# Performance work log

Hardware: AMD Instinct MI355X
Metric: run time of the kernel (lower is better)

The kernel has to match this reference:

```python
import jax, jax.numpy as jnp
import numpy as np

N, E, B = 50000, 800000, 1000
NODE_DIN, BB_DOUT, DHID, K = 32, 64, 64, 3
GLOB_DIN, EMBED_DIN = 64, 64
CIN = BB_DOUT + NODE_DIN  # 96


def setup_inputs() -> dict:
    key = jax.random.key(0)
    ks = jax.random.split(key, 24)

    def w(k, shape, fan_in):
        return jax.random.normal(k, shape, jnp.float32) / np.float32(np.sqrt(fan_in))

    inp = dict(
        x=jax.random.normal(ks[0], (N, NODE_DIN), jnp.float32),
        u=jax.random.normal(ks[1], (B, GLOB_DIN), jnp.float32),
        z=jax.random.normal(ks[2], (N, BB_DOUT), jnp.float32),
        edge_index=jax.random.randint(ks[3], (2, E), 0, N),
        edge_weight=jax.random.uniform(ks[4], (E,), jnp.float32),
        batch=jnp.sort(jax.random.randint(ks[5], (N,), 0, B)),
        batch_size=B,
        prev_h=jax.random.normal(ks[6], (N, DHID), jnp.float32),
    )
    # six ChebConvs of GConvGRU: x-convs take CIN, h-convs take DHID; all output DHID
    for i, nm in enumerate(["xz", "hz", "xr", "hr", "xh", "hh"]):
        cin = CIN if nm[0] == "x" else DHID
        inp[f"W{nm}"] = w(ks[7 + 2 * i], (K, cin, DHID), cin * K)
        inp[f"b{nm}"] = jnp.zeros((DHID,), jnp.float32)
    inp["Wg"] = w(ks[20], (GLOB_DIN, EMBED_DIN), GLOB_DIN)
    inp["bg"] = jnp.zeros((EMBED_DIN,), jnp.float32)
    return inp


def _cheb(xin, W, b, src, dst, w_norm, n):
    """ChebConv with sym norm, lambda_max=2 -> L_hat = -D^-1/2 A D^-1/2 (diag cancels)."""
    def prop(t):  # L_hat @ t  ([N,C])
        return -jax.ops.segment_sum(w_norm[:, None] * t[src], dst, num_segments=n)

    out = xin @ W[0] + b
    tx_prev = xin
    tx = None
    if W.shape[0] > 1:
        tx = prop(xin)
        out = out + tx @ W[1]
    for k in range(2, W.shape[0]):
        tx_new = 2.0 * prop(tx) - tx_prev
        out = out + tx_new @ W[k]
        tx_prev, tx = tx, tx_new
    return out


def reference(x, u, z, edge_index, edge_weight, batch, batch_size, prev_h,
              Wxz, bxz, Whz, bhz, Wxr, bxr, Whr, bhr, Wxh, bxh, Whh, bhh, Wg, bg):
    n = x.shape[0]
    src, dst = edge_index[0], edge_index[1]
    deg = jax.ops.segment_sum(edge_weight, src, num_segments=n)
    deg_safe = jnp.where(deg > 0, deg, 1.0)
    dinv = jnp.where(deg > 0, jax.lax.rsqrt(deg_safe), 0.0)
    w_norm = dinv[src] * edge_weight * dinv[dst]

    xin = jnp.concatenate([z, x], axis=-1)  # [N, CIN]
    Z = jax.nn.sigmoid(_cheb(xin, Wxz, bxz, src, dst, w_norm, n)
                       + _cheb(prev_h, Whz, bhz, src, dst, w_norm, n))
    R = jax.nn.sigmoid(_cheb(xin, Wxr, bxr, src, dst, w_norm, n)
                       + _cheb(prev_h, Whr, bhr, src, dst, w_norm, n))
    Ht = jnp.tanh(_cheb(xin, Wxh, bxh, src, dst, w_norm, n)
                  + _cheb(prev_h * R, Whh, bhh, src, dst, w_norm, n))
    h = Z * prev_h + (1.0 - Z) * Ht

    graph_emb = jax.ops.segment_sum(z, batch, num_segments=batch_size)  # [B, BB_DOUT]
    global_emb = jax.nn.relu(u @ Wg + bg)                                # [B, EMBED_DIN]
    fused = jnp.concatenate([graph_emb, global_emb], axis=-1)           # [B, 128]
    return fused, h
```

## Files before the change

kernel.cpp:

```cpp
#include <hip/hip_runtime.h>

#define NN 50000
#define EE 800000
#define BB 1000
#define NB 196
#define NR 5
#define RS 10496
#define NC 32
#define CHUNK 25000

#define BUILD2 31250
#define PACK2 408
#define FINBLKS 782

typedef unsigned short u16;
typedef __attribute__((ext_vector_type(8))) short bf16x8;
typedef __attribute__((ext_vector_type(4))) float f32x4;

static __device__ __forceinline__ u16 f2b(float f) {
    union { float f; unsigned u; } v;
    v.f = f;
    unsigned r = v.u + 0x7fffu + ((v.u >> 16) & 1u);
    return (u16)(r >> 16);
}

static __device__ __forceinline__ float b2f(short s) {
    union { unsigned u; float f; } c;
    c.u = ((unsigned)(u16)s) << 16;
    return c.f;
}

__global__ __launch_bounds__(512) void k_hist(
    const int* __restrict__ src, const int* __restrict__ dst,
    const float* __restrict__ ew, float* __restrict__ deg_p,
    int* __restrict__ cnt_p, int* __restrict__ ctr) {
    __shared__ float sdeg[RS];
    __shared__ unsigned scnt2[RS / 2];
    if (blockIdx.x == 0 && threadIdx.x == 0) atomicExch(ctr, 0);
    int r = blockIdx.x % NR;
    int c = blockIdx.x / NR;
    int base = r * RS;
    for (int i = threadIdx.x; i < RS; i += 512) sdeg[i] = 0.f;
    for (int i = threadIdx.x; i < RS / 2; i += 512) scnt2[i] = 0u;
    __syncthreads();
    int e0 = c * CHUNK;
    for (int j = threadIdx.x; j < CHUNK; j += 512) {
        int e = e0 + j;
        int s = src[e], d = dst[e];
        int sl = s - base, dl = d - base;
        if ((unsigned)sl < RS) atomicAdd(&sdeg[sl], ew[e]);
        if ((unsigned)dl < RS) atomicAdd(&scnt2[dl >> 1], (dl & 1) ? 65536u : 1u);
    }
    __syncthreads();
    int lim = (NN - base < RS) ? (NN - base) : RS;
    for (int i = threadIdx.x; i < lim; i += 512) {
        deg_p[(size_t)c * NN + base + i] = sdeg[i];
        cnt_p[(size_t)c * NN + base + i] = (int)((scnt2[i >> 1] >> ((i & 1) * 16)) & 0xffffu);
    }
}

__global__ __launch_bounds__(256) void k_scan_build(
    const int* __restrict__ cnt_p, const float* __restrict__ deg_p,
    int* __restrict__ cnt, int* __restrict__ cbase, float* __restrict__ dinv,
    int* __restrict__ bsum, int* __restrict__ ctr,
    const float* __restrict__ z, const float* __restrict__ x,
    const float* __restrict__ ph, u16* __restrict__ A0,
    const float* __restrict__ Wxz, const float* __restrict__ Wxr,
    const float* __restrict__ Wxh, const float* __restrict__ Whz,
    const float* __restrict__ Whr, const float* __restrict__ Whh,
    u16* __restrict__ Wp, u16* __restrict__ W3p) {
    if (blockIdx.x >= NB) {
        int bid = blockIdx.x - NB;
        if (bid < BUILD2) {
            int i = bid * 256 + threadIdx.x;
            int n = i / 160, c = i - n * 160;
            float v;
            if (c < 64) v = z[n * 64 + c];
            else if (c < 96) v = x[n * 32 + (c - 64)];
            else v = ph[n * 64 + (c - 96)];
            A0[(size_t)n * 160 + c] = f2b(v);
        } else {
            int idx = (bid - BUILD2) * 256 + threadIdx.x;
            if (idx < 15 * 12 * 512) {
                int j = idx & 7, l = (idx >> 3) & 63;
                int ct = (idx >> 9) % 12, s = (idx >> 9) / 12;
                int k = 32 * s + (l >> 4) * 8 + j;
                int g = ct >> 2;
                int c = 16 * (ct & 3) + (l & 15);
                int lvl = k / 160, kk = k - lvl * 160;
                float val;
                if (kk < 96) {
                    const float* W = (g == 0) ? Wxz : ((g == 1) ? Wxr : Wxh);
                    val = W[(lvl * 96 + kk) * 64 + c];
                } else if (g == 2) {
                    val = 0.f;
                } else {
                    const float* W = (g == 0) ? Whz : Whr;
                    val = W[(lvl * 64 + (kk - 96)) * 64 + c];
                }
                Wp[idx] = f2b(val);
            } else {
                int i2 = idx - 15 * 12 * 512;
                int j = i2 & 7, l = (i2 >> 3) & 63;
                int ct = (i2 >> 9) & 3, s = i2 >> 11;
                int k = 32 * s + (l >> 4) * 8 + j;
                int ki = k >> 6, kr = k & 63;
                int c = 16 * ct + (l & 15);
                W3p[i2] = f2b(Whh[(ki * 64 + kr) * 64 + c]);
            }
        }
        return;
    }
    __shared__ int s[256];
    int b = blockIdx.x;
    int i = b * 256 + threadIdx.x;
    int v = 0;
    float d = 0.f;
    if (i < NN) {
#pragma unroll
        for (int p = 0; p < NC; p++) v += cnt_p[(size_t)p * NN + i];
#pragma unroll
        for (int p = 0; p < NC; p++) d += deg_p[(size_t)p * NN + i];
        cnt[i] = v;
    }
    s[threadIdx.x] = v;
    __syncthreads();
    for (int off = 1; off < 256; off <<= 1) {
        int t = (threadIdx.x >= off) ? s[threadIdx.x - off] : 0;
        __syncthreads();
        s[threadIdx.x] += t;
        __syncthreads();
    }
    int incl = s[threadIdx.x];
    if (threadIdx.x == 255) atomicExch(&bsum[b], s[255]);
    __threadfence();
    if (threadIdx.x == 0) {
        atomicAdd(ctr, 1);
        while (atomicAdd(ctr, 0) < NB) __builtin_amdgcn_s_sleep(8);
    }
    __syncthreads();
    __threadfence();
    int pv = (threadIdx.x < b) ? atomicAdd(&bsum[threadIdx.x], 0) : 0;
    s[threadIdx.x] = pv;
    __syncthreads();
    for (int off = 128; off > 0; off >>= 1) {
        if (threadIdx.x < off) s[threadIdx.x] += s[threadIdx.x + off];
        __syncthreads();
    }
    int prefix = s[0];
    if (i < NN) {
        int run = prefix + incl - v;
        dinv[i] = d > 0.f ? rsqrtf(d) : 0.f;
#pragma unroll
        for (int c = 0; c < NC; c++) {
            cbase[(size_t)c * NN + i] = run;
            run += cnt_p[(size_t)c * NN + i];
        }
    }
}

__global__ __launch_bounds__(512) void k_scatter_rank(
    const int* __restrict__ src, const int* __restrict__ dst,
    const float* __restrict__ ew, const float* __restrict__ dinv,
    const int* __restrict__ cbase, uint2* __restrict__ csr8) {
    __shared__ unsigned rank2[RS / 2];
    int r = blockIdx.x % NR;
    int c = blockIdx.x / NR;
    int base = r * RS;
    for (int i = threadIdx.x; i < RS / 2; i += 512) rank2[i] = 0u;
    __syncthreads();
    int e0 = c * CHUNK;
    for (int j = threadIdx.x; j < CHUNK; j += 512) {
        int e = e0 + j;
        int d = dst[e];
        int dl = d - base;
        if ((unsigned)dl < RS) {
            int s = src[e];
            unsigned old = atomicAdd(&rank2[dl >> 1], (dl & 1) ? 65536u : 1u);
            int rank = (int)((old >> ((dl & 1) * 16)) & 0xffffu);
            int pos = cbase[(size_t)c * NN + d] + rank;
            float w = dinv[s] * ew[e] * dinv[d];
            csr8[pos] = make_uint2((unsigned)s, __float_as_uint(w));
        }
    }
}

template <int C, int SCALE, bool HB, int BS, int INS, int OUTS>
__global__ __launch_bounds__(BS) void k_pull(
    const u16* __restrict__ in, const u16* __restrict__ base, u16* __restrict__ out,
    const uint2* __restrict__ csr8, const int* __restrict__ row_ptr,
    const int* __restrict__ cnt) {
    constexpr int TPR = C / 16;
    int tid = blockIdx.x * BS + threadIdx.x;
    int r = tid / TPR;
    int c16 = (tid - r * TPR) * 16;
    if (r >= NN) return;
    int s0 = row_ptr[r], n = cnt[r];
    float acc[16];
#pragma unroll
    for (int k = 0; k < 16; k++) acc[k] = 0.f;
    const u16* inp = in + c16;
    uint2 e = (n > 0) ? csr8[s0] : make_uint2(0u, 0u);
    for (int j = 0; j < n; j++) {
        uint2 ec = e;
        if (j + 1 < n) e = csr8[s0 + j + 1];
        float w = __uint_as_float(ec.y);
        const u16* p = inp + (size_t)ec.x * INS;
        bf16x8 v0 = *(const bf16x8*)(p);
        bf16x8 v1 = *(const bf16x8*)(p + 8);
#pragma unroll
        for (int k = 0; k < 8; k++) {
            acc[k] += w * b2f(v0[k]);
            acc[8 + k] += w * b2f(v1[k]);
        }
    }
    const float sc = -(float)SCALE;
    float o[16];
    if (HB) {
        const u16* bp = base + (size_t)r * INS + c16;
        bf16x8 b0 = *(const bf16x8*)(bp);
        bf16x8 b1 = *(const bf16x8*)(bp + 8);
#pragma unroll
        for (int k = 0; k < 8; k++) {
            o[k] = sc * acc[k] - b2f(b0[k]);
            o[8 + k] = sc * acc[8 + k] - b2f(b1[k]);
        }
    } else {
#pragma unroll
        for (int k = 0; k < 16; k++) o[k] = sc * acc[k];
    }
    bf16x8 p0, p1;
#pragma unroll
    for (int k = 0; k < 8; k++) {
        p0[k] = (short)f2b(o[k]);
        p1[k] = (short)f2b(o[8 + k]);
    }
    u16* op = out + (size_t)r * OUTS + c16;
    *(bf16x8*)(op) = p0;
    *(bf16x8*)(op + 8) = p1;
}

__global__ __launch_bounds__(256) void k_gates_mfma(
    const u16* __restrict__ A0, const u16* __restrict__ A1, const u16* __restrict__ A2,
    const u16* __restrict__ Wp,
    const float* __restrict__ bxz, const float* __restrict__ bhz,
    const float* __restrict__ bxr, const float* __restrict__ bhr,
    const float* __restrict__ bxh,
    u16* __restrict__ Zb16, u16* __restrict__ Hx16, u16* __restrict__ A3) {
    int wv = (blockIdx.x * 256 + threadIdx.x) >> 6;
    int lane = threadIdx.x & 63;
    int r0 = wv * 16;
    if (r0 >= NN) return;
    int q = lane >> 4, j0 = lane & 15;

    f32x4 acc[12];
#pragma unroll
    for (int i = 0; i < 12; i++) acc[i] = (f32x4){0.f, 0.f, 0.f, 0.f};

    size_t rofs = (size_t)(r0 + j0) * 160 + q * 8;
    const u16* arow[3] = {A0 + rofs, A1 + rofs, A2 + rofs};
#pragma unroll
    for (int s = 0; s < 15; s++) {
        bf16x8 a = *(const bf16x8*)(arow[s / 5] + 32 * (s % 5));
        const u16* bp = Wp + (size_t)(s * 12) * 512 + lane * 8;
#pragma unroll
        for (int ct = 0; ct < 12; ct++) {
            bf16x8 b = *(const bf16x8*)(bp + ct * 512);
            acc[ct] = __builtin_amdgcn_mfma_f32_16x16x32_bf16(a, b, acc[ct], 0, 0, 0);
        }
    }

#pragma unroll
    for (int ct = 0; ct < 4; ct++) {
        int j = 16 * ct + j0;
        float bz = bxz[j] + bhz[j];
        float br = bxr[j] + bhr[j];
        float bh = bxh[j];
#pragma unroll
        for (int reg = 0; reg < 4; reg++) {
            int r = r0 + q * 4 + reg;
            size_t i = (size_t)r * 64 + j;
            float zp = acc[ct][reg] + bz;
            float rp = acc[ct + 4][reg] + br;
            float hp = acc[ct + 8][reg] + bh;
            float zv = 1.f / (1.f + expf(-zp));
            float rv = 1.f / (1.f + expf(-rp));
            float phv = b2f((short)A0[(size_t)r * 160 + 96 + j]);
            Zb16[i] = f2b(zv);
            Hx16[i] = f2b(hp);
            A3[(size_t)r * 192 + j] = f2b(rv * phv);
        }
    }
}

__global__ __launch_bounds__(256) void k_final_tail(
    const u16* __restrict__ A3, const u16* __restrict__ W3p,
    const float* __restrict__ bhh, const u16* __restrict__ Hx16,
    const u16* __restrict__ Zb16, const u16* __restrict__ A0,
    float* __restrict__ outh,
    const float* __restrict__ z, const int* __restrict__ batch,
    const float* __restrict__ u, const float* __restrict__ Wg,
    const float* __restrict__ bg, float* __restrict__ outF) {
    if (blockIdx.x >= FINBLKS) {
        int b = ((blockIdx.x - FINBLKS) * 256 + threadIdx.x) >> 6;
        int lane = threadIdx.x & 63;
        if (b >= BB) return;
        int lo = 0, hi = NN;
        while (lo < hi) {
            int m = (lo + hi) >> 1;
            if (batch[m] < b) lo = m + 1; else hi = m;
        }
        int start = lo;
        hi = NN;
        while (lo < hi) {
            int m = (lo + hi) >> 1;
            if (batch[m] < b + 1) lo = m + 1; else hi = m;
        }
        int end = lo;
        float acc = 0.f;
        for (int n = start; n < end; n++) acc += z[(size_t)n * 64 + lane];
        float g = bg[lane];
        const float* ur = u + (size_t)b * 64;
        for (int k = 0; k < 64; k++) g += ur[k] * Wg[k * 64 + lane];
        g = fmaxf(g, 0.f);
        outF[(size_t)b * 128 + lane] = acc;
        outF[(size_t)b * 128 + 64 + lane] = g;
        return;
    }
    int wv = (blockIdx.x * 256 + threadIdx.x) >> 6;
    int lane = threadIdx.x & 63;
    int r0 = wv * 16;
    if (r0 >= NN) return;
    int q = lane >> 4, j0 = lane & 15;

    f32x4 acc[4];
#pragma unroll
    for (int i = 0; i < 4; i++) acc[i] = (f32x4){0.f, 0.f, 0.f, 0.f};

    const u16* arow = A3 + (size_t)(r0 + j0) * 192 + q * 8;
#pragma unroll
    for (int s = 0; s < 6; s++) {
        bf16x8 a = *(const bf16x8*)(arow + 32 * s);
        const u16* bp = W3p + (size_t)(s * 4) * 512 + lane * 8;
#pragma unroll
        for (int ct = 0; ct < 4; ct++) {
            bf16x8 b = *(const bf16x8*)(bp + ct * 512);
            acc[ct] = __builtin_amdgcn_mfma_f32_16x16x32_bf16(a, b, acc[ct], 0, 0, 0);
        }
    }

#pragma unroll
    for (int ct = 0; ct < 4; ct++) {
        int j = 16 * ct + j0;
        float bh = bhh[j];
#pragma unroll
        for (int reg = 0; reg < 4; reg++) {
            int r = r0 + q * 4 + reg;
            size_t i = (size_t)r * 64 + j;
            float ht = tanhf(b2f((short)Hx16[i]) + acc[ct][reg] + bh);
            float zv = b2f((short)Zb16[i]);
            float phv = b2f((short)A0[(size_t)r * 160 + 96 + j]);
            outh[i] = zv * phv + (1.f - zv) * ht;
        }
    }
}

extern "C" void kernel_launch(void* const* d_in, const int* in_sizes, int n_in,
                              void* d_out, int out_size, void* d_ws, size_t ws_size,
                              hipStream_t stream) {
    const float* x  = (const float*)d_in[0];
    const float* u  = (const float*)d_in[1];
    const float* z  = (const float*)d_in[2];
    const int*   ei = (const int*)d_in[3];
    const float* ew = (const float*)d_in[4];
    const int* batch = (const int*)d_in[5];
    const float* ph = (const float*)d_in[7];
    const float *Wxz = (const float*)d_in[8],  *bxz = (const float*)d_in[9];
    const float *Whz = (const float*)d_in[10], *bhz = (const float*)d_in[11];
    const float *Wxr = (const float*)d_in[12], *bxr = (const float*)d_in[13];
    const float *Whr = (const float*)d_in[14], *bhr = (const float*)d_in[15];
    const float *Wxh = (const float*)d_in[16], *bxh = (const float*)d_in[17];
    const float *Whh = (const float*)d_in[18], *bhh = (const float*)d_in[19];
    const float *Wg  = (const float*)d_in[20], *bg  = (const float*)d_in[21];
    const int* src = ei;
    const int* dst = ei + EE;

    char* wsb = (char*)d_ws;
    size_t o = 0;
    auto alloc = [&](size_t bytes) {
        void* p = wsb + o;
        o += (bytes + 255) & ~(size_t)255;
        return p;
    };
    float* deg_p = (float*)alloc((size_t)NC * NN * 4);
    int*   cnt_p = (int*)alloc((size_t)NC * NN * 4);
    int*   cnt   = (int*)alloc(NN * 4);
    int*   cbase = (int*)alloc((size_t)NC * NN * 4);
    float* dinv  = (float*)alloc(NN * 4);
    int*   bsum  = (int*)alloc(256 * 4);
    int*   ctr   = (int*)alloc(256);
    uint2* csr8  = (uint2*)alloc((size_t)EE * 8);
    u16*   Zb16  = (u16*)alloc((size_t)NN * 64 * 2);
    u16*   Hx16  = (u16*)alloc((size_t)NN * 64 * 2);
    u16*   A0    = (u16*)alloc((size_t)NN * 160 * 2);
    u16*   A1    = (u16*)alloc((size_t)NN * 160 * 2);
    u16*   A2    = (u16*)alloc((size_t)NN * 160 * 2);
    u16*   A3    = (u16*)alloc((size_t)NN * 192 * 2);
    u16*   Wp    = (u16*)alloc(15 * 12 * 512 * 2);
    u16*   W3p   = (u16*)alloc(6 * 4 * 512 * 2);

    float* outF = (float*)d_out;
    float* outH = outF + (size_t)BB * 128;

    const int BLK = 256;
    const int gPull160 = (NN + 31) / 32;
    const int gPull64 = (NN + 63) / 64;
    const int gTail = (BB * 64 + BLK - 1) / BLK;
    int* row_ptr = cbase;

    k_hist<<<NR * NC, 512, 0, stream>>>(src, dst, ew, deg_p, cnt_p, ctr);

    k_scan_build<<<NB + BUILD2 + PACK2, 256, 0, stream>>>(
        cnt_p, deg_p, cnt, cbase, dinv, bsum, ctr,
        z, x, ph, A0, Wxz, Wxr, Wxh, Whz, Whr, Whh, Wp, W3p);

    k_scatter_rank<<<NR * NC, 512, 0, stream>>>(src, dst, ew, dinv, cbase, csr8);

    k_pull<160, 1, false, 320, 160, 160><<<gPull160, 320, 0, stream>>>(
        A0, nullptr, A1, csr8, row_ptr, cnt);
    k_pull<160, 2, true, 320, 160, 160><<<gPull160, 320, 0, stream>>>(
        A1, A0, A2, csr8, row_ptr, cnt);

    k_gates_mfma<<<FINBLKS, BLK, 0, stream>>>(A0, A1, A2, Wp, bxz, bhz, bxr, bhr, bxh,
                                              Zb16, Hx16, A3);

    k_pull<64, 1, false, 256, 192, 192><<<gPull64, 256, 0, stream>>>(
        A3, nullptr, A3 + 64, csr8, row_ptr, cnt);
    k_pull<64, 2, true, 256, 192, 192><<<gPull64, 256, 0, stream>>>(
        A3 + 64, A3, A3 + 128, csr8, row_ptr, cnt);

    k_final_tail<<<FINBLKS + gTail, BLK, 0, stream>>>(A3, W3p, bhh, Hx16, Zb16, A0, outH,
                                                      z, batch, u, Wg, bg, outF);
}
```

Measured before the change: 458.3 us.

## Fold Chebyshev recurrence into packed weights and split scan from build

The Chebyshev T2 = 2*L*T1 - T0 term is folded into the weights: W0' = W0 - W2 and W2' = 2*W2, so the second pull stores L*T1 directly and skips reading the base tensor and the fused scale/subtract. The combined scan/build kernel is split into a separate build kernel with 512-thread blocks and a separate scan kernel. The scan now keeps per-chunk counts in registers instead of reloading them from memory. The split adds one kernel launch, and dropping the co-scheduled build work may change how the spin barrier in the scan behaves. Folding the weights changes bf16 rounding slightly.

```diff
diff --git a/kernel.cpp b/kernel.cpp
--- a/kernel.cpp
+++ b/kernel.cpp
@@ -9,8 +9,8 @@
 #define NC 32
 #define CHUNK 25000
 
-#define BUILD2 31250
-#define PACK2 408
+#define BUILDBLKS 15625
+#define PACKBLKS 204
 #define FINBLKS 782
 
 typedef unsigned short u16;
@@ -59,68 +59,80 @@
     }
 }
 
-__global__ __launch_bounds__(256) void k_scan_build(
-    const int* __restrict__ cnt_p, const float* __restrict__ deg_p,
-    int* __restrict__ cnt, int* __restrict__ cbase, float* __restrict__ dinv,
-    int* __restrict__ bsum, int* __restrict__ ctr,
+__global__ __launch_bounds__(512) void k_build(
     const float* __restrict__ z, const float* __restrict__ x,
     const float* __restrict__ ph, u16* __restrict__ A0,
     const float* __restrict__ Wxz, const float* __restrict__ Wxr,
     const float* __restrict__ Wxh, const float* __restrict__ Whz,
     const float* __restrict__ Whr, const float* __restrict__ Whh,
     u16* __restrict__ Wp, u16* __restrict__ W3p) {
-    if (blockIdx.x >= NB) {
-        int bid = blockIdx.x - NB;
-        if (bid < BUILD2) {
-            int i = bid * 256 + threadIdx.x;
-            int n = i / 160, c = i - n * 160;
-            float v;
-            if (c < 64) v = z[n * 64 + c];
-            else if (c < 96) v = x[n * 32 + (c - 64)];
-            else v = ph[n * 64 + (c - 96)];
-            A0[(size_t)n * 160 + c] = f2b(v);
+    int bid = blockIdx.x;
+    if (bid < BUILDBLKS) {
+        int i = bid * 512 + threadIdx.x;
+        int n = i / 160, c = i - n * 160;
+        float v;
+        if (c < 64) v = z[n * 64 + c];
+        else if (c < 96) v = x[n * 32 + (c - 64)];
+        else v = ph[n * 64 + (c - 96)];
+        A0[(size_t)n * 160 + c] = f2b(v);
+        return;
+    }
+    int idx = (bid - BUILDBLKS) * 512 + threadIdx.x;
+    if (idx < 15 * 12 * 512) {
+        int j = idx & 7, l = (idx >> 3) & 63;
+        int ct = (idx >> 9) % 12, s = (idx >> 9) / 12;
+        int k = 32 * s + (l >> 4) * 8 + j;
+        int g = ct >> 2;
+        int c = 16 * (ct & 3) + (l & 15);
+        int lvl = k / 160, kk = k - lvl * 160;
+        float val;
+        if (kk < 96) {
+            const float* W = (g == 0) ? Wxz : ((g == 1) ? Wxr : Wxh);
+            if (lvl == 0)      val = W[kk * 64 + c] - W[(192 + kk) * 64 + c];
+            else if (lvl == 1) val = W[(96 + kk) * 64 + c];
+            else               val = 2.f * W[(192 + kk) * 64 + c];
+        } else if (g == 2) {
+            val = 0.f;
         } else {
-            int idx = (bid - BUILD2) * 256 + threadIdx.x;
-            if (idx < 15 * 12 * 512) {
-                int j = idx & 7, l = (idx >> 3) & 63;
-                int ct = (idx >> 9) % 12, s = (idx >> 9) / 12;
-                int k = 32 * s + (l >> 4) * 8 + j;
-                int g = ct >> 2;
-                int c = 16 * (ct & 3) + (l & 15);
-                int lvl = k / 160, kk = k - lvl * 160;
-                float val;
-                if (kk < 96) {
-                    const float* W = (g == 0) ? Wxz : ((g == 1) ? Wxr : Wxh);
-                    val = W[(lvl * 96 + kk) * 64 + c];
-                } else if (g == 2) {
-                    val = 0.f;
-                } else {
-                    const float* W = (g == 0) ? Whz : Whr;
-                    val = W[(lvl * 64 + (kk - 96)) * 64 + c];
-                }
-                Wp[idx] = f2b(val);
-            } else {
-                int i2 = idx - 15 * 12 * 512;
-                int j = i2 & 7, l = (i2 >> 3) & 63;
-                int ct = (i2 >> 9) & 3, s = i2 >> 11;
-                int k = 32 * s + (l >> 4) * 8 + j;
-                int ki = k >> 6, kr = k & 63;
-                int c = 16 * ct + (l & 15);
-                W3p[i2] = f2b(Whh[(ki * 64 + kr) * 64 + c]);
-            }
-        }
-        return;
-    }
+            const float* W = (g == 0) ? Whz : Whr;
+            int kh = kk - 96;
+            if (lvl == 0)      val = W[kh * 64 + c] - W[(128 + kh) * 64 + c];
+            else if (lvl == 1) val = W[(64 + kh) * 64 + c];
+            else               val = 2.f * W[(128 + kh) * 64 + c];
+        }
+        Wp[idx] = f2b(val);
+    } else {
+        int i2 = idx - 15 * 12 * 512;
+        int j = i2 & 7, l = (i2 >> 3) & 63;
+        int ct = (i2 >> 9) & 3, s = i2 >> 11;
+        int k = 32 * s + (l >> 4) * 8 + j;
+        int ki = k >> 6, kr = k & 63;
+        int c = 16 * ct + (l & 15);
+        float val;
+        if (ki == 0)      val = Whh[kr * 64 + c] - Whh[(128 + kr) * 64 + c];
+        else if (ki == 1) val = Whh[(64 + kr) * 64 + c];
+        else              val = 2.f * Whh[(128 + kr) * 64 + c];
+        W3p[i2] = f2b(val);
+    }
+}
+
+__global__ __launch_bounds__(256) void k_scan(
+    const int* __restrict__ cnt_p, const float* __restrict__ deg_p,
+    int* __restrict__ cnt, int* __restrict__ cbase, float* __restrict__ dinv,
+    int* __restrict__ bsum, int* __restrict__ ctr) {
     __shared__ int s[256];
     int b = blockIdx.x;
     int i = b * 256 + threadIdx.x;
+    int cp[NC];
     int v = 0;
     float d = 0.f;
     if (i < NN) {
 #pragma unroll
-        for (int p = 0; p < NC; p++) v += cnt_p[(size_t)p * NN + i];
-#pragma unroll
-        for (int p = 0; p < NC; p++) d += deg_p[(size_t)p * NN + i];
+        for (int p = 0; p < NC; p++) {
+            cp[p] = cnt_p[(size_t)p * NN + i];
+            v += cp[p];
+            d += deg_p[(size_t)p * NN + i];
+        }
         cnt[i] = v;
     }
     s[threadIdx.x] = v;
@@ -154,7 +166,7 @@
 #pragma unroll
         for (int c = 0; c < NC; c++) {
             cbase[(size_t)c * NN + i] = run;
-            run += cnt_p[(size_t)c * NN + i];
+            run += cp[c];
         }
     }
 }
@@ -185,9 +197,9 @@
     }
 }
 
-template <int C, int SCALE, bool HB, int BS, int INS, int OUTS>
+template <int C, int BS, int INS, int OUTS>
 __global__ __launch_bounds__(BS) void k_pull(
-    const u16* __restrict__ in, const u16* __restrict__ base, u16* __restrict__ out,
+    const u16* __restrict__ in, u16* __restrict__ out,
     const uint2* __restrict__ csr8, const int* __restrict__ row_ptr,
     const int* __restrict__ cnt) {
     constexpr int TPR = C / 16;
@@ -214,26 +226,11 @@
             acc[8 + k] += w * b2f(v1[k]);
         }
     }
-    const float sc = -(float)SCALE;
-    float o[16];
-    if (HB) {
-        const u16* bp = base + (size_t)r * INS + c16;
-        bf16x8 b0 = *(const bf16x8*)(bp);
-        bf16x8 b1 = *(const bf16x8*)(bp + 8);
-#pragma unroll
-        for (int k = 0; k < 8; k++) {
-            o[k] = sc * acc[k] - b2f(b0[k]);
-            o[8 + k] = sc * acc[8 + k] - b2f(b1[k]);
-        }
-    } else {
-#pragma unroll
-        for (int k = 0; k < 16; k++) o[k] = sc * acc[k];
-    }
     bf16x8 p0, p1;
 #pragma unroll
     for (int k = 0; k < 8; k++) {
-        p0[k] = (short)f2b(o[k]);
-        p1[k] = (short)f2b(o[8 + k]);
+        p0[k] = (short)f2b(-acc[k]);
+        p1[k] = (short)f2b(-acc[8 + k]);
     }
     u16* op = out + (size_t)r * OUTS + c16;
     *(bf16x8*)(op) = p0;
@@ -420,24 +417,21 @@
 
     k_hist<<<NR * NC, 512, 0, stream>>>(src, dst, ew, deg_p, cnt_p, ctr);
 
-    k_scan_build<<<NB + BUILD2 + PACK2, 256, 0, stream>>>(
-        cnt_p, deg_p, cnt, cbase, dinv, bsum, ctr,
+    k_build<<<BUILDBLKS + PACKBLKS, 512, 0, stream>>>(
         z, x, ph, A0, Wxz, Wxr, Wxh, Whz, Whr, Whh, Wp, W3p);
 
+    k_scan<<<NB, 256, 0, stream>>>(cnt_p, deg_p, cnt, cbase, dinv, bsum, ctr);
+
     k_scatter_rank<<<NR * NC, 512, 0, stream>>>(src, dst, ew, dinv, cbase, csr8);
 
-    k_pull<160, 1, false, 320, 160, 160><<<gPull160, 320, 0, stream>>>(
-        A0, nullptr, A1, csr8, row_ptr, cnt);
-    k_pull<160, 2, true, 320, 160, 160><<<gPull160, 320, 0, stream>>>(
-        A1, A0, A2, csr8, row_ptr, cnt);
+    k_pull<160, 320, 160, 160><<<gPull160, 320, 0, stream>>>(A0, A1, csr8, row_ptr, cnt);
+    k_pull<160, 320, 160, 160><<<gPull160, 320, 0, stream>>>(A1, A2, csr8, row_ptr, cnt);
 
     k_gates_mfma<<<FINBLKS, BLK, 0, stream>>>(A0, A1, A2, Wp, bxz, bhz, bxr, bhr, bxh,
                                               Zb16, Hx16, A3);
 
-    k_pull<64, 1, false, 256, 192, 192><<<gPull64, 256, 0, stream>>>(
-        A3, nullptr, A3 + 64, csr8, row_ptr, cnt);
-    k_pull<64, 2, true, 256, 192, 192><<<gPull64, 256, 0, stream>>>(
-        A3 + 64, A3, A3 + 128, csr8, row_ptr, cnt);
+    k_pull<64, 256, 192, 192><<<gPull64, 256, 0, stream>>>(A3, A3 + 64, csr8, row_ptr, cnt);
+    k_pull<64, 256, 192, 192><<<gPull64, 256, 0, stream>>>(A3 + 64, A3 + 128, csr8, row_ptr, cnt);
 
     k_final_tail<<<FINBLKS + gTail, BLK, 0, stream>>>(A3, W3p, bhh, Hx16, Zb16, A0, outH,
                                                       z, batch, u, Wg, bg, outF);
```

After: 449.3 us. 1.02x faster.
